# Optimization experiments

Measured on AMD Instinct MI355X. Metric: run time of the kernel, lower is better.

The kernel has to match this reference:

```python
import jax, jax.numpy as jnp
import numpy as np

N_NODES = 100000
N_EDGES = 3200000
R0, R1, R2, N1 = 16, 8, 16, 32


def setup_inputs() -> dict:
    key = jax.random.key(0)
    ks = jax.random.split(key, 12)
    x = jax.random.normal(ks[0], (N_NODES, R0), dtype=jnp.float32)
    edge_index = jax.random.randint(ks[1], (2, N_EDGES), 0, N_NODES, dtype=jnp.int64)
    s = 0.1
    return {
        "x": x,
        "edge_index": edge_index,
        # GraphConv 1: lin_rel (weight+bias) applied to aggregated neighbors, lin_root (no bias) to self
        "W_rel1": jax.random.normal(ks[2], (R0, R1), dtype=jnp.float32) * s,
        "b_rel1": jnp.zeros((R1,), dtype=jnp.float32),
        "W_root1": jax.random.normal(ks[3], (R0, R1), dtype=jnp.float32) * s,
        # GraphConv 2
        "W_rel2": jax.random.normal(ks[4], (R1, R2), dtype=jnp.float32) * s,
        "b_rel2": jnp.zeros((R2,), dtype=jnp.float32),
        "W_root2": jax.random.normal(ks[5], (R1, R2), dtype=jnp.float32) * s,
        # fc layers
        "W_fc1": jax.random.normal(ks[6], (R2, N1), dtype=jnp.float32) * s,
        "b_fc1": jnp.zeros((N1,), dtype=jnp.float32),
        "W_fc2": jax.random.normal(ks[7], (N1, 1), dtype=jnp.float32) * s,
        "b_fc2": jnp.zeros((1,), dtype=jnp.float32),
    }


def _graph_conv(x, src, dst, W_rel, b_rel, W_root):
    # GraphConv with aggr='add': out_i = lin_rel(sum_{j->i} x_j) + lin_root(x_i)
    agg = jax.ops.segment_sum(x[src], dst, num_segments=N_NODES)  # [N, d_in]
    return agg @ W_rel + b_rel + x @ W_root


def reference(x, edge_index,
              W_rel1, b_rel1, W_root1,
              W_rel2, b_rel2, W_root2,
              W_fc1, b_fc1, W_fc2, b_fc2):
    src, dst = edge_index[0], edge_index[1]
    h = jax.nn.relu(_graph_conv(x, src, dst, W_rel1, b_rel1, W_root1))
    h = jax.nn.relu(_graph_conv(h, src, dst, W_rel2, b_rel2, W_root2))
    h = jax.nn.relu(h @ W_fc1 + b_fc1)
    out = h @ W_fc2 + b_fc2  # [N, 1]
    return out - jnp.mean(out)
```

## Files before the change

kernel.cpp:

```cpp
#include <hip/hip_runtime.h>

#define NN 100000
#define NE 3200000
#define BSH 7
#define BNODES 128
#define NBUCK 782
#define BCAP 4800
#define BIN_CHUNK 8192
#define NBIN_BLOCKS ((NE + BIN_CHUNK - 1) / BIN_CHUNK)
#define NL1_BLOCKS ((NN + 1023) / 1024)

#define S1 2097152.0f
#define S2 524288.0f
#define INV_S1 (1.0f / S1)
#define INV_S2 (1.0f / S2)

__global__ __launch_bounds__(1024, 8) void bin_and_l1(
        const float* __restrict__ x,
        const float* __restrict__ Wrel1,
        const float* __restrict__ brel1,
        const float* __restrict__ Wroot1,
        const int* __restrict__ src,
        const int* __restrict__ dst,
        int* __restrict__ y1q,
        int* __restrict__ initq,
        int* __restrict__ bucketCnt,
        int* __restrict__ bpay) {
    int t = threadIdx.x;

    if (blockIdx.x >= NBIN_BLOCKS) {
        __shared__ float sW[16 * 8];
        __shared__ float sR[16 * 8];
        __shared__ float sb[8];
        if (t < 128) { sW[t] = Wrel1[t]; sR[t] = Wroot1[t]; }
        if (t < 8)   { sb[t] = brel1[t]; }
        __syncthreads();

        int i = (blockIdx.x - NBIN_BLOCKS) * 1024 + t;
        if (i >= NN) return;

        const float4* xp = (const float4*)(x + (size_t)i * 16);
        float4 x0 = xp[0], x1 = xp[1], x2 = xp[2], x3 = xp[3];
        float xi[16] = {x0.x, x0.y, x0.z, x0.w, x1.x, x1.y, x1.z, x1.w,
                        x2.x, x2.y, x2.z, x2.w, x3.x, x3.y, x3.z, x3.w};

        float y[8], r[8];
#pragma unroll
        for (int j = 0; j < 8; ++j) { y[j] = 0.0f; r[j] = sb[j]; }
#pragma unroll
        for (int k = 0; k < 16; ++k) {
            float xv = xi[k];
#pragma unroll
            for (int j = 0; j < 8; ++j) {
                y[j] = fmaf(xv, sW[k * 8 + j], y[j]);
                r[j] = fmaf(xv, sR[k * 8 + j], r[j]);
            }
        }
        int4* yp = (int4*)(y1q + (size_t)i * 8);
        int4* ap = (int4*)(initq + (size_t)i * 8);
        int4 q0, q1, p0, p1;
        q0.x = __float2int_rn(y[0] * S1); q0.y = __float2int_rn(y[1] * S1);
        q0.z = __float2int_rn(y[2] * S1); q0.w = __float2int_rn(y[3] * S1);
        q1.x = __float2int_rn(y[4] * S1); q1.y = __float2int_rn(y[5] * S1);
        q1.z = __float2int_rn(y[6] * S1); q1.w = __float2int_rn(y[7] * S1);
        p0.x = __float2int_rn(r[0] * S1); p0.y = __float2int_rn(r[1] * S1);
        p0.z = __float2int_rn(r[2] * S1); p0.w = __float2int_rn(r[3] * S1);
        p1.x = __float2int_rn(r[4] * S1); p1.y = __float2int_rn(r[5] * S1);
        p1.z = __float2int_rn(r[6] * S1); p1.w = __float2int_rn(r[7] * S1);
        yp[0] = q0; yp[1] = q1;
        ap[0] = p0; ap[1] = p1;
        return;
    }

    __shared__ int2 stage2[BIN_CHUNK];
    __shared__ int  hist[NBUCK];
    __shared__ int  gdelta[NBUCK];
    __shared__ int  wsum16[16];

    int e0 = blockIdx.x * BIN_CHUNK;
    int nE = NE - e0; if (nE > BIN_CHUNK) nE = BIN_CHUNK;
    int nv = nE >> 2;

    if (t < NBUCK) hist[t] = 0;
    __syncthreads();

    const int4* dst4 = (const int4*)(dst + e0);
    const int4* src4 = (const int4*)(src + e0);

    int4 d0_, s0_, d1_, s1_;
    bool h0 = (t < nv), h1 = (t + 1024 < nv);
    if (h0) {
        d0_ = dst4[t]; s0_ = src4[t];
        atomicAdd(&hist[d0_.x >> BSH], 1);
        atomicAdd(&hist[d0_.y >> BSH], 1);
        atomicAdd(&hist[d0_.z >> BSH], 1);
        atomicAdd(&hist[d0_.w >> BSH], 1);
    }
    if (h1) {
        d1_ = dst4[t + 1024]; s1_ = src4[t + 1024];
        atomicAdd(&hist[d1_.x >> BSH], 1);
        atomicAdd(&hist[d1_.y >> BSH], 1);
        atomicAdd(&hist[d1_.z >> BSH], 1);
        atomicAdd(&hist[d1_.w >> BSH], 1);
    }
    __syncthreads();

    int c = (t < NBUCK) ? hist[t] : 0;
    int lane = t & 63, w = t >> 6;
    int pref = c;
#pragma unroll
    for (int off = 1; off < 64; off <<= 1) {
        int u = __shfl_up(pref, off);
        if (lane >= off) pref += u;
    }
    if (lane == 63) wsum16[w] = pref;
    __syncthreads();
    if (t < 16) {
        int s = wsum16[t];
#pragma unroll
        for (int off = 1; off < 16; off <<= 1) {
            int u = __shfl_up(s, off);
            if (t >= off) s += u;
        }
        wsum16[t] = s;
    }
    __syncthreads();
    int base = w ? wsum16[w - 1] : 0;
    int excl = base + pref - c;

    if (t < NBUCK) {
        int gb0 = c ? atomicAdd(&bucketCnt[t], c) : 0;
        hist[t] = excl;
        gdelta[t] = t * BCAP + gb0 - excl;
    }
    __syncthreads();

#define PLACE1(dv, sv) do {                                              \
        int b_ = (dv) >> BSH;                                            \
        int r_ = atomicAdd(&hist[b_], 1);                                \
        int ga_ = r_ + gdelta[b_];                                       \
        int2 e_; e_.x = (((dv) & (BNODES - 1)) << 17) | (sv);            \
        e_.y = (ga_ < (b_ + 1) * BCAP) ? ga_ : -1;                       \
        stage2[r_] = e_;                                                 \
    } while (0)

    if (h0) { PLACE1(d0_.x, s0_.x); PLACE1(d0_.y, s0_.y);
              PLACE1(d0_.z, s0_.z); PLACE1(d0_.w, s0_.w); }
    if (h1) { PLACE1(d1_.x, s1_.x); PLACE1(d1_.y, s1_.y);
              PLACE1(d1_.z, s1_.z); PLACE1(d1_.w, s1_.w); }
#undef PLACE1
    __syncthreads();

    for (int p = t; p < nE; p += 1024) {
        int2 e = stage2[p];
        if (e.y >= 0) bpay[e.y] = e.x;
    }
}

__global__ __launch_bounds__(512, 8) void bucket_agg1(const int* __restrict__ bucketCnt,
                                                      const int* __restrict__ bpay,
                                                      const int* __restrict__ y1q,
                                                      int* __restrict__ h1q ) {
    __shared__ int qacc[BNODES * 8];
    int t = threadIdx.x;
    int b = blockIdx.x;
    int gb = b * BCAP;
    int fbase = b * (BNODES * 8);

    for (int k = t; k < BNODES * 8; k += 512) {
        int gi = fbase + k;
        qacc[k] = (gi < NN * 8) ? h1q[gi] : 0;
    }
    int C = bucketCnt[b]; if (C > BCAP) C = BCAP;
    __syncthreads();

    int f = t & 7, g = t >> 3;
    const int4* bp4 = (const int4*)(bpay + gb);
    int iters = C >> 9;
    for (int it = 0; it < iters; ++it) {
        int4 va = bp4[(it << 7) + (g << 1)];
        int4 vb = bp4[(it << 7) + (g << 1) + 1];
        int a0 = y1q[((va.x & 0x1FFFF) << 3) + f];
        int a1 = y1q[((va.y & 0x1FFFF) << 3) + f];
        int a2 = y1q[((va.z & 0x1FFFF) << 3) + f];
        int a3 = y1q[((va.w & 0x1FFFF) << 3) + f];
        int a4 = y1q[((vb.x & 0x1FFFF) << 3) + f];
        int a5 = y1q[((vb.y & 0x1FFFF) << 3) + f];
        int a6 = y1q[((vb.z & 0x1FFFF) << 3) + f];
        int a7 = y1q[((vb.w & 0x1FFFF) << 3) + f];
        atomicAdd(&qacc[((va.x >> 17) << 3) + f], a0);
        atomicAdd(&qacc[((va.y >> 17) << 3) + f], a1);
        atomicAdd(&qacc[((va.z >> 17) << 3) + f], a2);
        atomicAdd(&qacc[((va.w >> 17) << 3) + f], a3);
        atomicAdd(&qacc[((vb.x >> 17) << 3) + f], a4);
        atomicAdd(&qacc[((vb.y >> 17) << 3) + f], a5);
        atomicAdd(&qacc[((vb.z >> 17) << 3) + f], a6);
        atomicAdd(&qacc[((vb.w >> 17) << 3) + f], a7);
    }
    for (int e = (iters << 9) + g; e < C; e += 64) {
        int v = bpay[gb + e];
        int a = y1q[((v & 0x1FFFF) << 3) + f];
        atomicAdd(&qacc[((v >> 17) << 3) + f], a);
    }
    __syncthreads();

    for (int k = t; k < BNODES * 8; k += 512) {
        int gi = fbase + k;
        if (gi < NN * 8) {
            float h = (float)qacc[k] * INV_S1;
            h = h > 0.0f ? h : 0.0f;
            h1q[gi] = __float2int_rn(h * S2);
        }
    }
}

__global__ __launch_bounds__(512, 6) void bucket_agg2_tail(const int* __restrict__ bucketCnt,
                                                           const int* __restrict__ bpay,
                                                           const int* __restrict__ h1q,
                                                           const float* __restrict__ Wrel2,
                                                           const float* __restrict__ brel2,
                                                           const float* __restrict__ Wroot2,
                                                           const float* __restrict__ Wfc1,
                                                           const float* __restrict__ bfc1,
                                                           const float* __restrict__ Wfc2,
                                                           const float* __restrict__ bfc2,
                                                           float* __restrict__ out,
                                                           float* __restrict__ gsum) {
    __shared__ int qacc[BNODES * 8];
    __shared__ float sWrel2[128], sWroot2[128], sbrel2[16];
    __shared__ float sWfc1[512], sbfc1[32], sWfc2[32];
    __shared__ float sbfc2;
    __shared__ float wsum[8];

    int t = threadIdx.x;
    int b = blockIdx.x;
    int gb = b * BCAP;
    int n0 = b * BNODES;

    for (int k = t; k < BNODES * 8; k += 512) qacc[k] = 0;
    sWfc1[t] = Wfc1[t];
    if (t < 128) { sWrel2[t] = Wrel2[t]; sWroot2[t] = Wroot2[t]; }
    if (t >= 128 && t < 144) sbrel2[t - 128] = brel2[t - 128];
    if (t >= 192 && t < 224) { sbfc1[t - 192] = bfc1[t - 192]; sWfc2[t - 192] = Wfc2[t - 192]; }
    if (t == 256) sbfc2 = bfc2[0];
    int C = bucketCnt[b]; if (C > BCAP) C = BCAP;
    __syncthreads();

    int f = t & 7, g = t >> 3;
    const int4* bp4 = (const int4*)(bpay + gb);
    int iters = C >> 9;
    for (int it = 0; it < iters; ++it) {
        int4 va = bp4[(it << 7) + (g << 1)];
        int4 vb = bp4[(it << 7) + (g << 1) + 1];
        int a0 = h1q[((va.x & 0x1FFFF) << 3) + f];
        int a1 = h1q[((va.y & 0x1FFFF) << 3) + f];
        int a2 = h1q[((va.z & 0x1FFFF) << 3) + f];
        int a3 = h1q[((va.w & 0x1FFFF) << 3) + f];
        int a4 = h1q[((vb.x & 0x1FFFF) << 3) + f];
        int a5 = h1q[((vb.y & 0x1FFFF) << 3) + f];
        int a6 = h1q[((vb.z & 0x1FFFF) << 3) + f];
        int a7 = h1q[((vb.w & 0x1FFFF) << 3) + f];
        atomicAdd(&qacc[((va.x >> 17) << 3) + f], a0);
        atomicAdd(&qacc[((va.y >> 17) << 3) + f], a1);
        atomicAdd(&qacc[((va.z >> 17) << 3) + f], a2);
        atomicAdd(&qacc[((va.w >> 17) << 3) + f], a3);
        atomicAdd(&qacc[((vb.x >> 17) << 3) + f], a4);
        atomicAdd(&qacc[((vb.y >> 17) << 3) + f], a5);
        atomicAdd(&qacc[((vb.z >> 17) << 3) + f], a6);
        atomicAdd(&qacc[((vb.w >> 17) << 3) + f], a7);
    }
    for (int e = (iters << 9) + g; e < C; e += 64) {
        int v = bpay[gb + e];
        int a = h1q[((v & 0x1FFFF) << 3) + f];
        atomicAdd(&qacc[((v >> 17) << 3) + f], a);
    }
    __syncthreads();

    float o = 0.0f;
    int node = n0 + t;
    if (t < BNODES && node < NN) {
        const int4* hp = (const int4*)(h1q + (size_t)node * 8);
        int4 ha = hp[0], hb = hp[1];
        float h1v[8] = {ha.x * INV_S2, ha.y * INV_S2, ha.z * INV_S2, ha.w * INV_S2,
                        hb.x * INV_S2, hb.y * INV_S2, hb.z * INV_S2, hb.w * INV_S2};
        float s2[8];
#pragma unroll
        for (int j = 0; j < 8; ++j) s2[j] = (float)qacc[t * 8 + j] * INV_S2;

        float h2[16];
#pragma unroll
        for (int j = 0; j < 16; ++j) h2[j] = sbrel2[j];
#pragma unroll
        for (int k = 0; k < 8; ++k) {
            float sv = s2[k], hv = h1v[k];
#pragma unroll
            for (int j = 0; j < 16; ++j) {
                h2[j] = fmaf(sv, sWrel2[k * 16 + j], h2[j]);
                h2[j] = fmaf(hv, sWroot2[k * 16 + j], h2[j]);
            }
        }
#pragma unroll
        for (int j = 0; j < 16; ++j) h2[j] = h2[j] > 0.0f ? h2[j] : 0.0f;

        o = sbfc2;
#pragma unroll
        for (int m = 0; m < 32; ++m) {
            float a = sbfc1[m];
#pragma unroll
            for (int j = 0; j < 16; ++j) a = fmaf(h2[j], sWfc1[j * 32 + m], a);
            a = a > 0.0f ? a : 0.0f;
            o = fmaf(a, sWfc2[m], o);
        }
        out[node] = o;
    }

    float v = o;
#pragma unroll
    for (int off = 32; off > 0; off >>= 1) v += __shfl_down(v, off);
    int lane = t & 63, w = t >> 6;
    if (lane == 0) wsum[w] = v;
    __syncthreads();
    if (t == 0) {
        float s = 0.0f;
#pragma unroll
        for (int k = 0; k < 8; ++k) s += wsum[k];
        atomicAdd(gsum, s);
    }
}

__global__ void subtract_mean(float* __restrict__ out,
                              const float* __restrict__ gsum) {
    int i = blockIdx.x * blockDim.x + threadIdx.x;
    if (i < NN) out[i] -= (*gsum) * (1.0f / (float)NN);
}

extern "C" void kernel_launch(void* const* d_in, const int* in_sizes, int n_in,
                              void* d_out, int out_size, void* d_ws, size_t ws_size,
                              hipStream_t stream) {
    const float* x      = (const float*)d_in[0];
    const int*   ei     = (const int*)d_in[1];
    const float* Wrel1  = (const float*)d_in[2];
    const float* brel1  = (const float*)d_in[3];
    const float* Wroot1 = (const float*)d_in[4];
    const float* Wrel2  = (const float*)d_in[5];
    const float* brel2  = (const float*)d_in[6];
    const float* Wroot2 = (const float*)d_in[7];
    const float* Wfc1   = (const float*)d_in[8];
    const float* bfc1   = (const float*)d_in[9];
    const float* Wfc2   = (const float*)d_in[10];
    const float* bfc2   = (const float*)d_in[11];
    float* out = (float*)d_out;
    float* ws  = (float*)d_ws;

    int*   y1q       = (int*)ws;
    int*   h1q       = (int*)(ws + 800000);
    int*   bucketCnt = (int*)(ws + 1600000);
    float* gsum      = ws + 1600782;
    int*   bpay      = (int*)(ws + 1600783);

    const int* src = ei;
    const int* dst = ei + NE;

    hipMemsetAsync(bucketCnt, 0, (NBUCK + 1) * sizeof(int), stream);
    bin_and_l1<<<NBIN_BLOCKS + NL1_BLOCKS, 1024, 0, stream>>>(x, Wrel1, brel1, Wroot1,
                                                              src, dst, y1q, h1q,
                                                              bucketCnt, bpay);
    bucket_agg1<<<NBUCK, 512, 0, stream>>>(bucketCnt, bpay, y1q, h1q);
    bucket_agg2_tail<<<NBUCK, 512, 0, stream>>>(bucketCnt, bpay, h1q,
                                                Wrel2, brel2, Wroot2,
                                                Wfc1, bfc1, Wfc2, bfc2, out, gsum);
    subtract_mean<<<(NN + 255) / 256, 256, 0, stream>>>(out, gsum);
}
```

Baseline: 171.9 us.

## Split bucket aggregation across feature halves and separate dense tail kernel

Each edge bucket is now processed by two blocks, each handling four of the eight features, which doubles block count and halves shared accumulator size. Gathers are narrower per edge, but each block re-reads the full edge payload. The second aggregation writes raw sums to a scratch buffer (reusing y1q), and a new dense_tail kernel computes the MLP using all 512 threads per block instead of only 128 of 512. This adds a kernel launch and extra global traffic for the intermediate sums.

New measurement: 193.6 us. 1.13x slower.

```diff
diff --git a/kernel.cpp b/kernel.cpp
--- a/kernel.cpp
+++ b/kernel.cpp
@@ -9,6 +9,7 @@
 #define BIN_CHUNK 8192
 #define NBIN_BLOCKS ((NE + BIN_CHUNK - 1) / BIN_CHUNK)
 #define NL1_BLOCKS ((NN + 1023) / 1024)
+#define NAGG_BLOCKS 1568
 
 #define S1 2097152.0f
 #define S2 524288.0f
@@ -161,153 +162,175 @@
                                                       const int* __restrict__ bpay,
                                                       const int* __restrict__ y1q,
                                                       int* __restrict__ h1q ) {
-    __shared__ int qacc[BNODES * 8];
+    __shared__ int qacc[BNODES * 4];
     int t = threadIdx.x;
-    int b = blockIdx.x;
+    int j = blockIdx.x & 15, kk = blockIdx.x >> 4;
+    int b = (kk << 3) + (j & 7);
+    int fh4 = (j >> 3) << 2;
+    if (b >= NBUCK) return;
     int gb = b * BCAP;
     int fbase = b * (BNODES * 8);
 
-    for (int k = t; k < BNODES * 8; k += 512) {
-        int gi = fbase + k;
-        qacc[k] = (gi < NN * 8) ? h1q[gi] : 0;
+    {
+        int node = t >> 2, f = t & 3;
+        int gi = fbase + node * 8 + fh4 + f;
+        qacc[t] = (gi < NN * 8) ? h1q[gi] : 0;
     }
     int C = bucketCnt[b]; if (C > BCAP) C = BCAP;
     __syncthreads();
 
-    int f = t & 7, g = t >> 3;
+    int f = t & 3, g = t >> 2;
     const int4* bp4 = (const int4*)(bpay + gb);
-    int iters = C >> 9;
+    int iters = C >> 10;
     for (int it = 0; it < iters; ++it) {
-        int4 va = bp4[(it << 7) + (g << 1)];
-        int4 vb = bp4[(it << 7) + (g << 1) + 1];
-        int a0 = y1q[((va.x & 0x1FFFF) << 3) + f];
-        int a1 = y1q[((va.y & 0x1FFFF) << 3) + f];
-        int a2 = y1q[((va.z & 0x1FFFF) << 3) + f];
-        int a3 = y1q[((va.w & 0x1FFFF) << 3) + f];
-        int a4 = y1q[((vb.x & 0x1FFFF) << 3) + f];
-        int a5 = y1q[((vb.y & 0x1FFFF) << 3) + f];
-        int a6 = y1q[((vb.z & 0x1FFFF) << 3) + f];
-        int a7 = y1q[((vb.w & 0x1FFFF) << 3) + f];
-        atomicAdd(&qacc[((va.x >> 17) << 3) + f], a0);
-        atomicAdd(&qacc[((va.y >> 17) << 3) + f], a1);
-        atomicAdd(&qacc[((va.z >> 17) << 3) + f], a2);
-        atomicAdd(&qacc[((va.w >> 17) << 3) + f], a3);
-        atomicAdd(&qacc[((vb.x >> 17) << 3) + f], a4);
-        atomicAdd(&qacc[((vb.y >> 17) << 3) + f], a5);
-        atomicAdd(&qacc[((vb.z >> 17) << 3) + f], a6);
-        atomicAdd(&qacc[((vb.w >> 17) << 3) + f], a7);
-    }
-    for (int e = (iters << 9) + g; e < C; e += 64) {
+        int4 va = bp4[(it << 8) + (g << 1)];
+        int4 vb = bp4[(it << 8) + (g << 1) + 1];
+        int a0 = y1q[((va.x & 0x1FFFF) << 3) + fh4 + f];
+        int a1 = y1q[((va.y & 0x1FFFF) << 3) + fh4 + f];
+        int a2 = y1q[((va.z & 0x1FFFF) << 3) + fh4 + f];
+        int a3 = y1q[((va.w & 0x1FFFF) << 3) + fh4 + f];
+        int a4 = y1q[((vb.x & 0x1FFFF) << 3) + fh4 + f];
+        int a5 = y1q[((vb.y & 0x1FFFF) << 3) + fh4 + f];
+        int a6 = y1q[((vb.z & 0x1FFFF) << 3) + fh4 + f];
+        int a7 = y1q[((vb.w & 0x1FFFF) << 3) + fh4 + f];
+        atomicAdd(&qacc[((va.x >> 17) << 2) + f], a0);
+        atomicAdd(&qacc[((va.y >> 17) << 2) + f], a1);
+        atomicAdd(&qacc[((va.z >> 17) << 2) + f], a2);
+        atomicAdd(&qacc[((va.w >> 17) << 2) + f], a3);
+        atomicAdd(&qacc[((vb.x >> 17) << 2) + f], a4);
+        atomicAdd(&qacc[((vb.y >> 17) << 2) + f], a5);
+        atomicAdd(&qacc[((vb.z >> 17) << 2) + f], a6);
+        atomicAdd(&qacc[((vb.w >> 17) << 2) + f], a7);
+    }
+    for (int e = (iters << 10) + g; e < C; e += 128) {
         int v = bpay[gb + e];
-        int a = y1q[((v & 0x1FFFF) << 3) + f];
-        atomicAdd(&qacc[((v >> 17) << 3) + f], a);
-    }
-    __syncthreads();
-
-    for (int k = t; k < BNODES * 8; k += 512) {
-        int gi = fbase + k;
+        int a = y1q[((v & 0x1FFFF) << 3) + fh4 + f];
+        atomicAdd(&qacc[((v >> 17) << 2) + f], a);
+    }
+    __syncthreads();
+
+    {
+        int node = t >> 2, fo = t & 3;
+        int gi = fbase + node * 8 + fh4 + fo;
         if (gi < NN * 8) {
-            float h = (float)qacc[k] * INV_S1;
+            float h = (float)qacc[t] * INV_S1;
             h = h > 0.0f ? h : 0.0f;
             h1q[gi] = __float2int_rn(h * S2);
         }
     }
 }
 
-__global__ __launch_bounds__(512, 6) void bucket_agg2_tail(const int* __restrict__ bucketCnt,
-                                                           const int* __restrict__ bpay,
-                                                           const int* __restrict__ h1q,
-                                                           const float* __restrict__ Wrel2,
-                                                           const float* __restrict__ brel2,
-                                                           const float* __restrict__ Wroot2,
-                                                           const float* __restrict__ Wfc1,
-                                                           const float* __restrict__ bfc1,
-                                                           const float* __restrict__ Wfc2,
-                                                           const float* __restrict__ bfc2,
-                                                           float* __restrict__ out,
-                                                           float* __restrict__ gsum) {
-    __shared__ int qacc[BNODES * 8];
+__global__ __launch_bounds__(512, 8) void bucket_agg2(const int* __restrict__ bucketCnt,
+                                                      const int* __restrict__ bpay,
+                                                      const int* __restrict__ h1q,
+                                                      int* __restrict__ sagg) {
+    __shared__ int qacc[BNODES * 4];
+    int t = threadIdx.x;
+    int j = blockIdx.x & 15, kk = blockIdx.x >> 4;
+    int b = (kk << 3) + (j & 7);
+    int fh4 = (j >> 3) << 2;
+    if (b >= NBUCK) return;
+    int gb = b * BCAP;
+    int fbase = b * (BNODES * 8);
+
+    qacc[t] = 0;
+    int C = bucketCnt[b]; if (C > BCAP) C = BCAP;
+    __syncthreads();
+
+    int f = t & 3, g = t >> 2;
+    const int4* bp4 = (const int4*)(bpay + gb);
+    int iters = C >> 10;
+    for (int it = 0; it < iters; ++it) {
+        int4 va = bp4[(it << 8) + (g << 1)];
+        int4 vb = bp4[(it << 8) + (g << 1) + 1];
+        int a0 = h1q[((va.x & 0x1FFFF) << 3) + fh4 + f];
+        int a1 = h1q[((va.y & 0x1FFFF) << 3) + fh4 + f];
+        int a2 = h1q[((va.z & 0x1FFFF) << 3) + fh4 + f];
+        int a3 = h1q[((va.w & 0x1FFFF) << 3) + fh4 + f];
+        int a4 = h1q[((vb.x & 0x1FFFF) << 3) + fh4 + f];
+        int a5 = h1q[((vb.y & 0x1FFFF) << 3) + fh4 + f];
+        int a6 = h1q[((vb.z & 0x1FFFF) << 3) + fh4 + f];
+        int a7 = h1q[((vb.w & 0x1FFFF) << 3) + fh4 + f];
+        atomicAdd(&qacc[((va.x >> 17) << 2) + f], a0);
+        atomicAdd(&qacc[((va.y >> 17) << 2) + f], a1);
+        atomicAdd(&qacc[((va.z >> 17) << 2) + f], a2);
+        atomicAdd(&qacc[((va.w >> 17) << 2) + f], a3);
+        atomicAdd(&qacc[((vb.x >> 17) << 2) + f], a4);
+        atomicAdd(&qacc[((vb.y >> 17) << 2) + f], a5);
+        atomicAdd(&qacc[((vb.z >> 17) << 2) + f], a6);
+        atomicAdd(&qacc[((vb.w >> 17) << 2) + f], a7);
+    }
+    for (int e = (iters << 10) + g; e < C; e += 128) {
+        int v = bpay[gb + e];
+        int a = h1q[((v & 0x1FFFF) << 3) + fh4 + f];
+        atomicAdd(&qacc[((v >> 17) << 2) + f], a);
+    }
+    __syncthreads();
+
+    {
+        int node = t >> 2, fo = t & 3;
+        int gi = fbase + node * 8 + fh4 + fo;
+        if (gi < NN * 8) sagg[gi] = qacc[t];
+    }
+}
+
+__global__ __launch_bounds__(512) void dense_tail(const int* __restrict__ h1q,
+                                                  const int* __restrict__ sagg,
+                                                  const float* __restrict__ Wrel2,
+                                                  const float* __restrict__ brel2,
+                                                  const float* __restrict__ Wroot2,
+                                                  const float* __restrict__ Wfc1,
+                                                  const float* __restrict__ bfc1,
+                                                  const float* __restrict__ Wfc2,
+                                                  const float* __restrict__ bfc2,
+                                                  float* __restrict__ out,
+                                                  float* __restrict__ gsum) {
     __shared__ float sWrel2[128], sWroot2[128], sbrel2[16];
     __shared__ float sWfc1[512], sbfc1[32], sWfc2[32];
     __shared__ float sbfc2;
     __shared__ float wsum[8];
 
     int t = threadIdx.x;
-    int b = blockIdx.x;
-    int gb = b * BCAP;
-    int n0 = b * BNODES;
-
-    for (int k = t; k < BNODES * 8; k += 512) qacc[k] = 0;
     sWfc1[t] = Wfc1[t];
     if (t < 128) { sWrel2[t] = Wrel2[t]; sWroot2[t] = Wroot2[t]; }
     if (t >= 128 && t < 144) sbrel2[t - 128] = brel2[t - 128];
     if (t >= 192 && t < 224) { sbfc1[t - 192] = bfc1[t - 192]; sWfc2[t - 192] = Wfc2[t - 192]; }
     if (t == 256) sbfc2 = bfc2[0];
-    int C = bucketCnt[b]; if (C > BCAP) C = BCAP;
-    __syncthreads();
-
-    int f = t & 7, g = t >> 3;
-    const int4* bp4 = (const int4*)(bpay + gb);
-    int iters = C >> 9;
-    for (int it = 0; it < iters; ++it) {
-        int4 va = bp4[(it << 7) + (g << 1)];
-        int4 vb = bp4[(it << 7) + (g << 1) + 1];
-        int a0 = h1q[((va.x & 0x1FFFF) << 3) + f];
-        int a1 = h1q[((va.y & 0x1FFFF) << 3) + f];
-        int a2 = h1q[((va.z & 0x1FFFF) << 3) + f];
-        int a3 = h1q[((va.w & 0x1FFFF) << 3) + f];
-        int a4 = h1q[((vb.x & 0x1FFFF) << 3) + f];
-        int a5 = h1q[((vb.y & 0x1FFFF) << 3) + f];
-        int a6 = h1q[((vb.z & 0x1FFFF) << 3) + f];
-        int a7 = h1q[((vb.w & 0x1FFFF) << 3) + f];
-        atomicAdd(&qacc[((va.x >> 17) << 3) + f], a0);
-        atomicAdd(&qacc[((va.y >> 17) << 3) + f], a1);
-        atomicAdd(&qacc[((va.z >> 17) << 3) + f], a2);
-        atomicAdd(&qacc[((va.w >> 17) << 3) + f], a3);
-        atomicAdd(&qacc[((vb.x >> 17) << 3) + f], a4);
-        atomicAdd(&qacc[((vb.y >> 17) << 3) + f], a5);
-        atomicAdd(&qacc[((vb.z >> 17) << 3) + f], a6);
-        atomicAdd(&qacc[((vb.w >> 17) << 3) + f], a7);
-    }
-    for (int e = (iters << 9) + g; e < C; e += 64) {
-        int v = bpay[gb + e];
-        int a = h1q[((v & 0x1FFFF) << 3) + f];
-        atomicAdd(&qacc[((v >> 17) << 3) + f], a);
-    }
-    __syncthreads();
-
+    __syncthreads();
+
+    int node = blockIdx.x * 512 + t;
     float o = 0.0f;
-    int node = n0 + t;
-    if (t < BNODES && node < NN) {
+    if (node < NN) {
         const int4* hp = (const int4*)(h1q + (size_t)node * 8);
+        const int4* sp = (const int4*)(sagg + (size_t)node * 8);
         int4 ha = hp[0], hb = hp[1];
+        int4 sa = sp[0], sb = sp[1];
         float h1v[8] = {ha.x * INV_S2, ha.y * INV_S2, ha.z * INV_S2, ha.w * INV_S2,
                         hb.x * INV_S2, hb.y * INV_S2, hb.z * INV_S2, hb.w * INV_S2};
-        float s2[8];
-#pragma unroll
-        for (int j = 0; j < 8; ++j) s2[j] = (float)qacc[t * 8 + j] * INV_S2;
+        float s2[8]  = {sa.x * INV_S2, sa.y * INV_S2, sa.z * INV_S2, sa.w * INV_S2,
+                        sb.x * INV_S2, sb.y * INV_S2, sb.z * INV_S2, sb.w * INV_S2};
 
         float h2[16];
 #pragma unroll
-        for (int j = 0; j < 16; ++j) h2[j] = sbrel2[j];
+        for (int jj = 0; jj < 16; ++jj) h2[jj] = sbrel2[jj];
 #pragma unroll
         for (int k = 0; k < 8; ++k) {
             float sv = s2[k], hv = h1v[k];
 #pragma unroll
-            for (int j = 0; j < 16; ++j) {
-                h2[j] = fmaf(sv, sWrel2[k * 16 + j], h2[j]);
-                h2[j] = fmaf(hv, sWroot2[k * 16 + j], h2[j]);
+            for (int jj = 0; jj < 16; ++jj) {
+                h2[jj] = fmaf(sv, sWrel2[k * 16 + jj], h2[jj]);
+                h2[jj] = fmaf(hv, sWroot2[k * 16 + jj], h2[jj]);
             }
         }
 #pragma unroll
-        for (int j = 0; j < 16; ++j) h2[j] = h2[j] > 0.0f ? h2[j] : 0.0f;
+        for (int jj = 0; jj < 16; ++jj) h2[jj] = h2[jj] > 0.0f ? h2[jj] : 0.0f;
 
         o = sbfc2;
 #pragma unroll
         for (int m = 0; m < 32; ++m) {
             float a = sbfc1[m];
 #pragma unroll
-            for (int j = 0; j < 16; ++j) a = fmaf(h2[j], sWfc1[j * 32 + m], a);
+            for (int jj = 0; jj < 16; ++jj) a = fmaf(h2[jj], sWfc1[jj * 32 + m], a);
             a = a > 0.0f ? a : 0.0f;
             o = fmaf(a, sWfc2[m], o);
         }
@@ -357,6 +380,7 @@
     int*   bucketCnt = (int*)(ws + 1600000);
     float* gsum      = ws + 1600782;
     int*   bpay      = (int*)(ws + 1600783);
+    int*   sagg      = y1q;
 
     const int* src = ei;
     const int* dst = ei + NE;
@@ -365,9 +389,10 @@
     bin_and_l1<<<NBIN_BLOCKS + NL1_BLOCKS, 1024, 0, stream>>>(x, Wrel1, brel1, Wroot1,
                                                               src, dst, y1q, h1q,
                                                               bucketCnt, bpay);
-    bucket_agg1<<<NBUCK, 512, 0, stream>>>(bucketCnt, bpay, y1q, h1q);
-    bucket_agg2_tail<<<NBUCK, 512, 0, stream>>>(bucketCnt, bpay, h1q,
-                                                Wrel2, brel2, Wroot2,
-                                                Wfc1, bfc1, Wfc2, bfc2, out, gsum);
+    bucket_agg1<<<NAGG_BLOCKS, 512, 0, stream>>>(bucketCnt, bpay, y1q, h1q);
+    bucket_agg2<<<NAGG_BLOCKS, 512, 0, stream>>>(bucketCnt, bpay, h1q, sagg);
+    dense_tail<<<(NN + 511) / 512, 512, 0, stream>>>(h1q, sagg,
+                                                     Wrel2, brel2, Wroot2,
+                                                     Wfc1, bfc1, Wfc2, bfc2, out, gsum);
     subtract_mean<<<(NN + 255) / 256, 256, 0, stream>>>(out, gsum);
 }
```
